# Optimization experiments

Hardware: AMD Instinct MI355X
Metric: run time of the kernel (lower is better)

## Reference

```python
import jax, jax.numpy as jnp
import numpy as np
import math

D_MODEL = 1024
N_HEAD = 16
D_K = D_MODEL // N_HEAD
B, S = 2, 2048


def setup_inputs() -> dict:
    key = jax.random.key(0)
    ks = jax.random.split(key, 9)
    sc = 0.02
    return {
        "x": jax.random.normal(ks[0], (B, S, D_MODEL), dtype=jnp.float32),
        "Wq": jax.random.normal(ks[1], (D_MODEL, D_MODEL), dtype=jnp.float32) * sc,
        "bq": jnp.zeros((D_MODEL,), dtype=jnp.float32),
        "Wk": jax.random.normal(ks[2], (D_MODEL, D_MODEL), dtype=jnp.float32) * sc,
        "bk": jnp.zeros((D_MODEL,), dtype=jnp.float32),
        "Wv": jax.random.normal(ks[3], (D_MODEL, D_MODEL), dtype=jnp.float32) * sc,
        "bv": jnp.zeros((D_MODEL,), dtype=jnp.float32),
        "Wo": jax.random.normal(ks[4], (D_MODEL, D_MODEL), dtype=jnp.float32) * sc,
        "bo": jnp.zeros((D_MODEL,), dtype=jnp.float32),
    }


def reference(x, Wq, bq, Wk, bk, Wv, bv, Wo, bo):
    # cache=None prefill path: q_start=0, k_len=S (S <= MAX_CACHE_LEN)
    b, s, d = x.shape
    # projections (torch Linear: x @ W.T + b)
    q = (x @ Wq.T + bq).reshape(b, s, N_HEAD, D_K).transpose(0, 2, 1, 3)  # [b,h,s,dk]
    k = (x @ Wk.T + bk).reshape(b, s, N_HEAD, D_K).transpose(0, 2, 1, 3)
    v = (x @ Wv.T + bv).reshape(b, s, N_HEAD, D_K).transpose(0, 2, 1, 3)
    scores = jnp.einsum("bhqd,bhkd->bhqk", q, k) / math.sqrt(D_K)
    causal = jnp.triu(jnp.ones((s, s), dtype=bool), k=1)  # True above diagonal
    scores = jnp.where(causal[None, None], -jnp.inf, scores)
    attn = jax.nn.softmax(scores, axis=-1)  # dropout p=0 (eval)
    ctx = jnp.einsum("bhqk,bhkd->bhqd", attn, v)
    ctx = ctx.transpose(0, 2, 1, 3).reshape(b, s, d)
    return ctx @ Wo.T + bo
```

## Files before the change

### kernel.cpp

```cpp
#include <hip/hip_runtime.h>
#include <hip/hip_bf16.h>

#define DM 1024
#define NH 16
#define DK 64
#define BB 2
#define SS 2048
#define NTOK (BB*SS)
#define SCALE_LOG2E 0.1803368801111204f

typedef __attribute__((ext_vector_type(8))) short bf16x8;
typedef __attribute__((ext_vector_type(4))) float f32x4;
typedef __attribute__((ext_vector_type(4))) unsigned short us4;
typedef __attribute__((ext_vector_type(4))) unsigned int u32x4;

#define GLOAD16(gp, lp) \
  __builtin_amdgcn_global_load_lds((const __attribute__((address_space(1))) void*)(gp), \
                                   (__attribute__((address_space(3))) void*)(lp), 16, 0, 0)

__device__ inline unsigned short f2b(float f) {
  unsigned int x = __float_as_uint(f);
  return (unsigned short)((x + 0x7FFFu + ((x >> 16) & 1u)) >> 16);
}
__device__ inline unsigned int pack2bf(float a, float b) {
  unsigned int r;
  asm("v_cvt_pk_bf16_f32 %0, %1, %2" : "=v"(r) : "v"(a), "v"(b));
  return r;
}

#define XC4 (NTOK*DM/4)
#define WC4 (DM*DM/4)
__global__ void cast_all(const float* __restrict__ x,  const float* __restrict__ wq,
                         const float* __restrict__ wk, const float* __restrict__ wv,
                         const float* __restrict__ wo,
                         unsigned short* __restrict__ xb,  unsigned short* __restrict__ wqb,
                         unsigned short* __restrict__ wkb, unsigned short* __restrict__ wvb,
                         unsigned short* __restrict__ wob) {
  const int total = XC4 + 4*WC4;
  int i = blockIdx.x * blockDim.x + threadIdx.x;
  int stride = gridDim.x * blockDim.x;
  for (; i < total; i += stride) {
    const float* s; unsigned short* d; int off;
    if (i < XC4) { s = x; d = xb; off = i; }
    else {
      int j = i - XC4;
      int sel = j >> 18;
      off = j & (WC4 - 1);
      if      (sel == 0) { s = wq; d = wqb; }
      else if (sel == 1) { s = wk; d = wkb; }
      else if (sel == 2) { s = wv; d = wvb; }
      else               { s = wo; d = wob; }
    }
    float4 v = reinterpret_cast<const float4*>(s)[off];
    us4 o;
    o[0] = f2b(v.x); o[1] = f2b(v.y); o[2] = f2b(v.z); o[3] = f2b(v.w);
    reinterpret_cast<us4*>(d)[off] = o;
  }
}

__device__ __forceinline__ void gemm_mainloop(const unsigned short* __restrict__ A,
                                              const unsigned short* __restrict__ W,
                                              unsigned short* As, unsigned short* Bs,
                                              int m0, int n0, int tid, f32x4 acc[4][4]) {
  const int lane = tid & 63;
  const int w = tid >> 6;
  const int wr = w >> 1, wc = w & 1;
  const int g = lane >> 4, q = lane & 15;

  const int col0 = (((lane & 7) ^ ((lane >> 3) & 7)) << 3);
  const unsigned short* Ag = A + (size_t)(m0 + w*32 + (lane >> 3)) * DM + col0;
  const unsigned short* Bg = W + (size_t)(n0 + w*32 + (lane >> 3)) * DM + col0;
  char* AsB = (char*)As + w * 4096;
  char* BsB = (char*)Bs + w * 4096;

  const int fso = ((g ^ (q & 7)) << 4);

  for (int kt = 0; kt < DM; kt += 64) {
    __syncthreads();
    GLOAD16(Ag + kt,          AsB);
    GLOAD16(Ag + kt +  8*DM,  AsB + 1024);
    GLOAD16(Ag + kt + 16*DM,  AsB + 2048);
    GLOAD16(Ag + kt + 24*DM,  AsB + 3072);
    GLOAD16(Bg + kt,          BsB);
    GLOAD16(Bg + kt +  8*DM,  BsB + 1024);
    GLOAD16(Bg + kt + 16*DM,  BsB + 2048);
    GLOAD16(Bg + kt + 24*DM,  BsB + 3072);
    __syncthreads();
    #pragma unroll
    for (int h = 0; h < 2; h++) {
      const int so = fso ^ (h << 6);
      bf16x8 aF[4], bF[4];
      #pragma unroll
      for (int mt = 0; mt < 4; mt++)
        aF[mt] = *reinterpret_cast<const bf16x8*>((char*)As + (wr*64 + mt*16 + q)*128 + so);
      #pragma unroll
      for (int nt = 0; nt < 4; nt++)
        bF[nt] = *reinterpret_cast<const bf16x8*>((char*)Bs + (wc*64 + nt*16 + q)*128 + so);
      #pragma unroll
      for (int mt = 0; mt < 4; mt++)
        #pragma unroll
        for (int nt = 0; nt < 4; nt++)
          acc[mt][nt] = __builtin_amdgcn_mfma_f32_16x16x32_bf16(aF[mt], bF[nt], acc[mt][nt], 0, 0, 0);
    }
  }
}

__global__ __launch_bounds__(256, 2)
void gemm_qkv(const unsigned short* __restrict__ xb,
              const unsigned short* __restrict__ wqb, const unsigned short* __restrict__ wkb,
              const unsigned short* __restrict__ wvb,
              const float* __restrict__ bq, const float* __restrict__ bk,
              const float* __restrict__ bv,
              unsigned short* __restrict__ qo, unsigned short* __restrict__ ko,
              unsigned short* __restrict__ vto) {
  __shared__ unsigned short As[128*64];
  __shared__ unsigned short Bs[128*64];
  const int z = blockIdx.z;
  const unsigned short* W = (z == 0) ? wqb : (z == 1) ? wkb : wvb;
  const float* bias = (z == 0) ? bq : (z == 1) ? bk : bv;
  const int m0 = blockIdx.y * 128, n0 = blockIdx.x * 128;

  f32x4 acc[4][4];
  #pragma unroll
  for (int i = 0; i < 4; i++)
    #pragma unroll
    for (int j = 0; j < 4; j++)
      #pragma unroll
      for (int e = 0; e < 4; e++) acc[i][j][e] = 0.f;

  gemm_mainloop(xb, W, As, Bs, m0, n0, threadIdx.x, acc);

  const int lane = threadIdx.x & 63, w = threadIdx.x >> 6;
  const int wr = w >> 1, wc = w & 1, g = lane >> 4, q = lane & 15;
  const float sc = (z == 0) ? SCALE_LOG2E : 1.0f;
  #pragma unroll
  for (int mt = 0; mt < 4; mt++) {
    #pragma unroll
    for (int nt = 0; nt < 4; nt++) {
      const int mg0 = m0 + wr*64 + mt*16 + 4*g;
      const int ng  = n0 + wc*64 + nt*16 + q;
      const float bv_ = bias[ng];
      const int h = ng >> 6, d = ng & 63;
      if (z == 2) {
        const int b = mg0 >> 11, s = mg0 & 2047;
        us4 pk;
        #pragma unroll
        for (int r = 0; r < 4; r++) pk[r] = f2b(acc[mt][nt][r] + bv_);
        *reinterpret_cast<us4*>(&vto[((size_t)((b*NH + h)*DK + d)) * SS + s]) = pk;
      } else {
        unsigned short* out = (z == 0) ? qo : ko;
        #pragma unroll
        for (int r = 0; r < 4; r++) {
          const int m = mg0 + r;
          const int b = m >> 11, s = m & 2047;
          out[((size_t)((b*NH + h)*SS + s)) * DK + d] = f2b((acc[mt][nt][r] + bv_) * sc);
        }
      }
    }
  }
}

__global__ __launch_bounds__(256, 2)
void gemm_out(const unsigned short* __restrict__ ctx,
              const unsigned short* __restrict__ wob,
              const float* __restrict__ bo, float* __restrict__ out) {
  __shared__ unsigned short As[128*64];
  __shared__ unsigned short Bs[128*64];
  const int m0 = blockIdx.y * 128, n0 = blockIdx.x * 128;
  f32x4 acc[4][4];
  #pragma unroll
  for (int i = 0; i < 4; i++)
    #pragma unroll
    for (int j = 0; j < 4; j++)
      #pragma unroll
      for (int e = 0; e < 4; e++) acc[i][j][e] = 0.f;

  gemm_mainloop(ctx, wob, As, Bs, m0, n0, threadIdx.x, acc);

  const int lane = threadIdx.x & 63, w = threadIdx.x >> 6;
  const int wr = w >> 1, wc = w & 1, g = lane >> 4, q = lane & 15;
  #pragma unroll
  for (int mt = 0; mt < 4; mt++) {
    #pragma unroll
    for (int nt = 0; nt < 4; nt++) {
      const int mg0 = m0 + wr*64 + mt*16 + 4*g;
      const int ng  = n0 + wc*64 + nt*16 + q;
      const float bv_ = bo[ng];
      #pragma unroll
      for (int r = 0; r < 4; r++)
        out[(size_t)(mg0 + r) * DM + ng] = acc[mt][nt][r] + bv_;
    }
  }
}

__global__ __launch_bounds__(256, 2)
void attn_fwd(const unsigned short* __restrict__ Q,
              const unsigned short* __restrict__ Kg,
              const unsigned short* __restrict__ VT,
              unsigned short* __restrict__ ctx) {
  __shared__ float CMB[2][64][66];
  __shared__ float CML[2][64];
  const int qblk = (int)gridDim.y - 1 - (int)blockIdx.y;
  const int bh = blockIdx.x;
  const int tid = threadIdx.x;
  const int lane = tid & 63;
  const int w = tid >> 6;
  const int g = lane >> 4;
  const int q = lane & 15;
  const int q0 = qblk * 64;
  const int T = qblk + 1;
  const size_t base = (size_t)bh * SS * DK;

  bf16x8 aQ[4][2];
  #pragma unroll
  for (int rg = 0; rg < 4; rg++) {
    const unsigned short* qp = Q + base + (size_t)(q0 + rg*16 + q) * DK + g*8;
    aQ[rg][0] = *reinterpret_cast<const bf16x8*>(qp);
    aQ[rg][1] = *reinterpret_cast<const bf16x8*>(qp + 32);
  }

  f32x4 o[4][4];
  float l_run[4];
  #pragma unroll
  for (int rg = 0; rg < 4; rg++) {
    #pragma unroll
    for (int dt = 0; dt < 4; dt++)
      #pragma unroll
      for (int r = 0; r < 4; r++) o[rg][dt][r] = 0.f;
    l_run[rg] = 0.f;
  }

  const int src0 = q + 32*(g & 1);
  const int src1 = src0 + 16;
  const bool gsel = (g >> 1);

  bf16x8 aK[4][2], aV[4][2];
  if (w < T) {
    #pragma unroll
    for (int f = 0; f < 4; f++) {
      const unsigned short* kp = Kg + base + (size_t)(w*64 + f*16 + q) * DK + g*8;
      aK[f][0] = *reinterpret_cast<const bf16x8*>(kp);
      aK[f][1] = *reinterpret_cast<const bf16x8*>(kp + 32);
    }
    #pragma unroll
    for (int dt = 0; dt < 4; dt++) {
      const unsigned short* vp = VT + base + (size_t)(dt*16 + q) * SS + w*64 + g*8;
      aV[dt][0] = *reinterpret_cast<const bf16x8*>(vp);
      aV[dt][1] = *reinterpret_cast<const bf16x8*>(vp + 32);
    }
  }

  for (int t = w; t < T; t += 4) {
    const bool tail = (t == T - 1);
    #pragma unroll
    for (int rg = 0; rg < 4; rg++) {
      f32x4 sf[4];
      __builtin_amdgcn_s_setprio(1);
      #pragma unroll
      for (int f = 0; f < 4; f++) {
        f32x4 z;
        #pragma unroll
        for (int r = 0; r < 4; r++) z[r] = 0.f;
        z = __builtin_amdgcn_mfma_f32_16x16x32_bf16(aK[f][0], aQ[rg][0], z, 0, 0, 0);
        z = __builtin_amdgcn_mfma_f32_16x16x32_bf16(aK[f][1], aQ[rg][1], z, 0, 0, 0);
        sf[f] = z;
      }
      __builtin_amdgcn_s_setprio(0);

      if (rg == 3 && t + 4 < T) {
        #pragma unroll
        for (int f = 0; f < 4; f++) {
          const unsigned short* kp = Kg + base + (size_t)((t+4)*64 + f*16 + q) * DK + g*8;
          aK[f][0] = *reinterpret_cast<const bf16x8*>(kp);
          aK[f][1] = *reinterpret_cast<const bf16x8*>(kp + 32);
        }
      }

      const int grow = q0 + rg*16 + q;
      float p[4][4];
      float ps = 0.f;
      #pragma unroll
      for (int f = 0; f < 4; f++)
        #pragma unroll
        for (int r = 0; r < 4; r++) {
          float v = sf[f][r];
          if (tail) {
            int gcol = t*64 + f*16 + 4*g + r;
            if (gcol > grow) v = -1e30f;
          }
          float e = exp2f(v);
          p[f][r] = e;
          ps += e;
        }
      ps += __shfl_xor(ps, 16);
      ps += __shfl_xor(ps, 32);
      l_run[rg] += ps;

      unsigned int pk[4][2];
      #pragma unroll
      for (int f = 0; f < 4; f++) {
        pk[f][0] = pack2bf(p[f][0], p[f][1]);
        pk[f][1] = pack2bf(p[f][2], p[f][3]);
      }

      u32x4 bl, bh2;
      #pragma unroll
      for (int t2 = 0; t2 < 4; t2++) {
        const int src = (t2 < 2) ? src0 : src1;
        unsigned int s0 = (unsigned int)__shfl((int)pk[0][t2 & 1], src);
        unsigned int s1 = (unsigned int)__shfl((int)pk[1][t2 & 1], src);
        unsigned int s2 = (unsigned int)__shfl((int)pk[2][t2 & 1], src);
        unsigned int s3 = (unsigned int)__shfl((int)pk[3][t2 & 1], src);
        bl[t2]  = gsel ? s1 : s0;
        bh2[t2] = gsel ? s3 : s2;
      }
      bf16x8 Blo = __builtin_bit_cast(bf16x8, bl);
      bf16x8 Bhi = __builtin_bit_cast(bf16x8, bh2);

      __builtin_amdgcn_s_setprio(1);
      #pragma unroll
      for (int dt = 0; dt < 4; dt++) {
        o[rg][dt] = __builtin_amdgcn_mfma_f32_16x16x32_bf16(aV[dt][0], Blo, o[rg][dt], 0, 0, 0);
        o[rg][dt] = __builtin_amdgcn_mfma_f32_16x16x32_bf16(aV[dt][1], Bhi, o[rg][dt], 0, 0, 0);
      }
      __builtin_amdgcn_s_setprio(0);
    }

    if (t + 4 < T) {
      #pragma unroll
      for (int dt = 0; dt < 4; dt++) {
        const unsigned short* vp = VT + base + (size_t)(dt*16 + q) * SS + (t+4)*64 + g*8;
        aV[dt][0] = *reinterpret_cast<const bf16x8*>(vp);
        aV[dt][1] = *reinterpret_cast<const bf16x8*>(vp + 32);
      }
    }
  }

  if (w >= 2) {
    const int slot = w - 2;
    #pragma unroll
    for (int rg = 0; rg < 4; rg++) {
      #pragma unroll
      for (int dt = 0; dt < 4; dt++)
        #pragma unroll
        for (int r = 0; r < 4; r++)
          CMB[slot][rg*16 + q][dt*16 + 4*g + r] = o[rg][dt][r];
      CML[slot][rg*16 + q] = l_run[rg];
    }
  }
  __syncthreads();
  if (w < 2) {
    const int slot = w;
    #pragma unroll
    for (int rg = 0; rg < 4; rg++) {
      l_run[rg] += CML[slot][rg*16 + q];
      #pragma unroll
      for (int dt = 0; dt < 4; dt++)
        #pragma unroll
        for (int r = 0; r < 4; r++)
          o[rg][dt][r] += CMB[slot][rg*16 + q][dt*16 + 4*g + r];
    }
  }
  __syncthreads();
  if (w == 1) {
    #pragma unroll
    for (int rg = 0; rg < 4; rg++) {
      #pragma unroll
      for (int dt = 0; dt < 4; dt++)
        #pragma unroll
        for (int r = 0; r < 4; r++)
          CMB[0][rg*16 + q][dt*16 + 4*g + r] = o[rg][dt][r];
      CML[0][rg*16 + q] = l_run[rg];
    }
  }
  __syncthreads();
  if (w == 0) {
    const int b = bh >> 4, h = bh & 15;
    #pragma unroll
    for (int rg = 0; rg < 4; rg++) {
      float lfin = l_run[rg] + CML[0][rg*16 + q];
      const float inv = 1.0f / lfin;
      const int s = q0 + rg*16 + q;
      #pragma unroll
      for (int dt = 0; dt < 4; dt++) {
        us4 pkv;
        #pragma unroll
        for (int r = 0; r < 4; r++) {
          float val = o[rg][dt][r] + CMB[0][rg*16 + q][dt*16 + 4*g + r];
          pkv[r] = f2b(val * inv);
        }
        *reinterpret_cast<us4*>(&ctx[((size_t)(b*SS + s)) * DM + h*DK + dt*16 + 4*g]) = pkv;
      }
    }
  }
}

extern "C" void kernel_launch(void* const* d_in, const int* in_sizes, int n_in,
                              void* d_out, int out_size, void* d_ws, size_t ws_size,
                              hipStream_t stream) {
  const float* x  = (const float*)d_in[0];
  const float* Wq = (const float*)d_in[1];
  const float* bq = (const float*)d_in[2];
  const float* Wk = (const float*)d_in[3];
  const float* bk = (const float*)d_in[4];
  const float* Wv = (const float*)d_in[5];
  const float* bv = (const float*)d_in[6];
  const float* Wo = (const float*)d_in[7];
  const float* bo = (const float*)d_in[8];
  float* out = (float*)d_out;

  unsigned short* xb  = (unsigned short*)d_ws;
  unsigned short* wqb = xb  + (size_t)NTOK * DM;
  unsigned short* wkb = wqb + (size_t)DM * DM;
  unsigned short* wvb = wkb + (size_t)DM * DM;
  unsigned short* wob = wvb + (size_t)DM * DM;
  unsigned short* q   = wob + (size_t)DM * DM;
  unsigned short* k   = q   + (size_t)NTOK * DM;
  unsigned short* vt  = k   + (size_t)NTOK * DM;
  unsigned short* ctx = vt  + (size_t)NTOK * DM;

  cast_all<<<2048, 256, 0, stream>>>(x, Wq, Wk, Wv, Wo, xb, wqb, wkb, wvb, wob);

  gemm_qkv<<<dim3(DM/128, NTOK/128, 3), 256, 0, stream>>>(xb, wqb, wkb, wvb,
                                                          bq, bk, bv, q, k, vt);

  attn_fwd<<<dim3(BB*NH, SS/64), 256, 0, stream>>>(q, k, vt, ctx);

  gemm_out<<<dim3(DM/128, NTOK/128), 256, 0, stream>>>(ctx, wob, bo, out);
}
```

Before: 112.9 us.

## Split long causal attention rows into two KV chunks with merge kernel

Query blocks 16-31 now have their KV range split across two workgroups, each covering up to 16 KV tiles. Each workgroup writes an unnormalized bf16 partial output and its row sums to scratch space that reuses the x-bf16 buffer. A new merge kernel adds the two partials and normalizes them. The aim is to even out the causal workload imbalance and shorten the tail. The cost is an extra launch, extra global traffic for the partials, and bf16 rounding of the partials before they are merged. The merge skips max rescaling, which assumes both chunks share a fixed softmax reference, as the original kernel appears to do.

Result: slower. 120.2 us (+6.5%).

```diff
diff --git a/kernel.cpp b/kernel.cpp
--- a/kernel.cpp
+++ b/kernel.cpp
@@ -21,6 +21,9 @@
 __device__ inline unsigned short f2b(float f) {
   unsigned int x = __float_as_uint(f);
   return (unsigned short)((x + 0x7FFFu + ((x >> 16) & 1u)) >> 16);
+}
+__device__ inline float b2f(unsigned short u) {
+  return __uint_as_float(((unsigned int)u) << 16);
 }
 __device__ inline unsigned int pack2bf(float a, float b) {
   unsigned int r;
@@ -197,10 +200,16 @@
 void attn_fwd(const unsigned short* __restrict__ Q,
               const unsigned short* __restrict__ Kg,
               const unsigned short* __restrict__ VT,
-              unsigned short* __restrict__ ctx) {
+              unsigned short* __restrict__ ctx,
+              unsigned short* __restrict__ pob,
+              float* __restrict__ plf) {
   __shared__ float CMB[2][64][66];
   __shared__ float CML[2][64];
-  const int qblk = (int)gridDim.y - 1 - (int)blockIdx.y;
+  const int y = blockIdx.y;
+  int qblk, chunk;
+  if (y < 16)      { qblk = 16 + y;        chunk = 0; }
+  else if (y < 32) { qblk = 31 - (y - 16); chunk = 1; }
+  else             { qblk = 15 - (y - 32); chunk = 0; }
   const int bh = blockIdx.x;
   const int tid = threadIdx.x;
   const int lane = tid & 63;
@@ -209,6 +218,8 @@
   const int q = lane & 15;
   const int q0 = qblk * 64;
   const int T = qblk + 1;
+  const int t0 = chunk << 4;
+  const int t1 = (T < t0 + 16) ? T : (t0 + 16);
   const size_t base = (size_t)bh * SS * DK;
 
   bf16x8 aQ[4][2];
@@ -235,22 +246,22 @@
   const bool gsel = (g >> 1);
 
   bf16x8 aK[4][2], aV[4][2];
-  if (w < T) {
+  if (t0 + w < t1) {
     #pragma unroll
     for (int f = 0; f < 4; f++) {
-      const unsigned short* kp = Kg + base + (size_t)(w*64 + f*16 + q) * DK + g*8;
+      const unsigned short* kp = Kg + base + (size_t)((t0 + w)*64 + f*16 + q) * DK + g*8;
       aK[f][0] = *reinterpret_cast<const bf16x8*>(kp);
       aK[f][1] = *reinterpret_cast<const bf16x8*>(kp + 32);
     }
     #pragma unroll
     for (int dt = 0; dt < 4; dt++) {
-      const unsigned short* vp = VT + base + (size_t)(dt*16 + q) * SS + w*64 + g*8;
+      const unsigned short* vp = VT + base + (size_t)(dt*16 + q) * SS + (t0 + w)*64 + g*8;
       aV[dt][0] = *reinterpret_cast<const bf16x8*>(vp);
       aV[dt][1] = *reinterpret_cast<const bf16x8*>(vp + 32);
     }
   }
 
-  for (int t = w; t < T; t += 4) {
+  for (int t = t0 + w; t < t1; t += 4) {
     const bool tail = (t == T - 1);
     #pragma unroll
     for (int rg = 0; rg < 4; rg++) {
@@ -267,7 +278,7 @@
       }
       __builtin_amdgcn_s_setprio(0);
 
-      if (rg == 3 && t + 4 < T) {
+      if (rg == 3 && t + 4 < t1) {
         #pragma unroll
         for (int f = 0; f < 4; f++) {
           const unsigned short* kp = Kg + base + (size_t)((t+4)*64 + f*16 + q) * DK + g*8;
@@ -326,7 +337,7 @@
       __builtin_amdgcn_s_setprio(0);
     }
 
-    if (t + 4 < T) {
+    if (t + 4 < t1) {
       #pragma unroll
       for (int dt = 0; dt < 4; dt++) {
         const unsigned short* vp = VT + base + (size_t)(dt*16 + q) * SS + (t+4)*64 + g*8;
@@ -375,24 +386,66 @@
   }
   __syncthreads();
   if (w == 0) {
-    const int b = bh >> 4, h = bh & 15;
-    #pragma unroll
-    for (int rg = 0; rg < 4; rg++) {
-      float lfin = l_run[rg] + CML[0][rg*16 + q];
-      const float inv = 1.0f / lfin;
-      const int s = q0 + rg*16 + q;
-      #pragma unroll
-      for (int dt = 0; dt < 4; dt++) {
-        us4 pkv;
-        #pragma unroll
-        for (int r = 0; r < 4; r++) {
-          float val = o[rg][dt][r] + CMB[0][rg*16 + q][dt*16 + 4*g + r];
-          pkv[r] = f2b(val * inv);
+    if (qblk >= 16) {
+      const int sidx = (bh*16 + (qblk - 16))*2 + chunk;
+      unsigned short* po = pob + (size_t)sidx * 4096;
+      float* pl = plf + (size_t)sidx * 64;
+      #pragma unroll
+      for (int rg = 0; rg < 4; rg++) {
+        float lfin = l_run[rg] + CML[0][rg*16 + q];
+        if (g == 0) pl[rg*16 + q] = lfin;
+        #pragma unroll
+        for (int dt = 0; dt < 4; dt++) {
+          us4 pkv;
+          #pragma unroll
+          for (int r = 0; r < 4; r++)
+            pkv[r] = f2b(o[rg][dt][r] + CMB[0][rg*16 + q][dt*16 + 4*g + r]);
+          *reinterpret_cast<us4*>(&po[(rg*16 + q)*64 + dt*16 + 4*g]) = pkv;
         }
-        *reinterpret_cast<us4*>(&ctx[((size_t)(b*SS + s)) * DM + h*DK + dt*16 + 4*g]) = pkv;
-      }
-    }
-  }
+      }
+    } else {
+      const int b = bh >> 4, h = bh & 15;
+      #pragma unroll
+      for (int rg = 0; rg < 4; rg++) {
+        float lfin = l_run[rg] + CML[0][rg*16 + q];
+        const float inv = 1.0f / lfin;
+        const int s = q0 + rg*16 + q;
+        #pragma unroll
+        for (int dt = 0; dt < 4; dt++) {
+          us4 pkv;
+          #pragma unroll
+          for (int r = 0; r < 4; r++) {
+            float val = o[rg][dt][r] + CMB[0][rg*16 + q][dt*16 + 4*g + r];
+            pkv[r] = f2b(val * inv);
+          }
+          *reinterpret_cast<us4*>(&ctx[((size_t)(b*SS + s)) * DM + h*DK + dt*16 + 4*g]) = pkv;
+        }
+      }
+    }
+  }
+}
+
+__global__ void attn_merge(const unsigned short* __restrict__ pob,
+                           const float* __restrict__ plf,
+                           unsigned short* __restrict__ ctx) {
+  const int i = blockIdx.x * blockDim.x + threadIdx.x;
+  const int bhq = i >> 10;
+  const int rem = i & 1023;
+  const int row = rem >> 4;
+  const int c4 = (rem & 15) << 2;
+  const size_t s0 = (size_t)(bhq*2) * 4096;
+  const us4 a  = *reinterpret_cast<const us4*>(&pob[s0 + row*64 + c4]);
+  const us4 b_ = *reinterpret_cast<const us4*>(&pob[s0 + 4096 + row*64 + c4]);
+  const float l = plf[(bhq*2)*64 + row] + plf[(bhq*2 + 1)*64 + row];
+  const float inv = 1.0f / l;
+  const int bh = bhq >> 4, qb16 = bhq & 15;
+  const int b = bh >> 4, h = bh & 15;
+  const int s = (16 + qb16)*64 + row;
+  us4 o;
+  #pragma unroll
+  for (int j = 0; j < 4; j++)
+    o[j] = f2b((b2f(a[j]) + b2f(b_[j])) * inv);
+  *reinterpret_cast<us4*>(&ctx[((size_t)(b*SS + s)) * DM + h*DK + c4]) = o;
 }
 
 extern "C" void kernel_launch(void* const* d_in, const int* in_sizes, int n_in,
@@ -419,12 +472,16 @@
   unsigned short* vt  = k   + (size_t)NTOK * DM;
   unsigned short* ctx = vt  + (size_t)NTOK * DM;
 
+  unsigned short* pob = xb;
+  float* plf = (float*)(xb + (size_t)1024 * 4096);
+
   cast_all<<<2048, 256, 0, stream>>>(x, Wq, Wk, Wv, Wo, xb, wqb, wkb, wvb, wob);
 
   gemm_qkv<<<dim3(DM/128, NTOK/128, 3), 256, 0, stream>>>(xb, wqb, wkb, wvb,
                                                           bq, bk, bv, q, k, vt);
 
-  attn_fwd<<<dim3(BB*NH, SS/64), 256, 0, stream>>>(q, k, vt, ctx);
+  attn_fwd<<<dim3(BB*NH, 48), 256, 0, stream>>>(q, k, vt, ctx, pob, plf);
+  attn_merge<<<2048, 256, 0, stream>>>(pob, plf, ctx);
 
   gemm_out<<<dim3(DM/128, NTOK/128), 256, 0, stream>>>(ctx, wob, bo, out);
 }
```
